# Optimization experiments

Measured on AMD Instinct MI355X. Metric: run time of the kernel, lower is better.

Reference implementation:

```python
import jax, jax.numpy as jnp
import numpy as np

N = 8192
IN_F = 512
OUT_F = 256
EDGE_P = 0.02  # adjacency density


def setup_inputs() -> dict:
    key = jax.random.key(0)
    k1, k2, k3, k4 = jax.random.split(key, 4)
    x = jax.random.normal(k1, (N, IN_F), dtype=jnp.float32)
    # xavier_uniform with gain=1.414 ~ std gain*sqrt(2/(fan_in+fan_out))
    W = jax.random.normal(k2, (IN_F, OUT_F), dtype=jnp.float32) * (1.414 * np.sqrt(2.0 / (IN_F + OUT_F)))
    a = jax.random.normal(k3, (2 * OUT_F, 1), dtype=jnp.float32) * (1.414 * np.sqrt(2.0 / (2 * OUT_F + 1)))
    adj = (jax.random.uniform(k4, (N, N)) < EDGE_P).astype(jnp.float32)
    return {"x": x, "adj": adj, "W": W, "a": a}


def reference(x, adj, W, a):
    h = x @ W                        # [N, F]
    F = h.shape[1]
    # repeat/cat reduces to an outer sum of two [N] vectors.
    s_src = (h @ a[:F]).squeeze(-1)  # [N], contribution of h_i
    s_dst = (h @ a[F:]).squeeze(-1)  # [N], contribution of h_j
    e = jax.nn.leaky_relu(s_src[:, None] + s_dst[None, :], negative_slope=0.2)  # [N, N]
    # NOTE: original code softmaxes over the FULL row, THEN multiplies by adj.
    attention = jax.nn.softmax(e, axis=1) * adj  # [N, N]
    h_prime = attention @ h                      # [N, F]
    return h_prime, attention
```

## Files before the change

### kernel.cpp

```cpp
#include <hip/hip_runtime.h>
#include <hip/hip_bf16.h>

#define N_NODES 8192
#define IN_F    512
#define OUT_F   256
#define MAXNZ   512

#define BM 64
#define BN 64
#define BK 32

typedef float v4f __attribute__((ext_vector_type(4)));

__global__ __launch_bounds__(256) void k_gemm_h(const float* __restrict__ x,
                                                const float* __restrict__ W,
                                                float* __restrict__ h) {
  __shared__ float As[BK][BM + 4];
  __shared__ float Bs[BK][BN];
  const int t  = threadIdx.x;
  const int bm = blockIdx.x >> 2;
  const int bn = blockIdx.x & 3;
  const int m0 = bm * BM, n0 = bn * BN;
  const int tm = (t >> 4) * 4;
  const int tn = (t & 15) * 4;

  float acc[4][4] = {{0.f, 0.f, 0.f, 0.f}, {0.f, 0.f, 0.f, 0.f},
                     {0.f, 0.f, 0.f, 0.f}, {0.f, 0.f, 0.f, 0.f}};

  for (int k0 = 0; k0 < IN_F; k0 += BK) {
#pragma unroll
    for (int i = 0; i < 2; ++i) {
      const int fi = t + i * 256;
      const int ar = fi >> 3;
      const int ac = (fi & 7) << 2;
      const float4 va = *(const float4*)&x[(size_t)(m0 + ar) * IN_F + k0 + ac];
      As[ac + 0][ar] = va.x;
      As[ac + 1][ar] = va.y;
      As[ac + 2][ar] = va.z;
      As[ac + 3][ar] = va.w;
      const int br = fi >> 4;
      const int bc = (fi & 15) << 2;
      *(float4*)&Bs[br][bc] = *(const float4*)&W[(size_t)(k0 + br) * OUT_F + n0 + bc];
    }
    __syncthreads();
#pragma unroll
    for (int k = 0; k < BK; ++k) {
      const float4 a = *(const float4*)&As[k][tm];
      const float4 b = *(const float4*)&Bs[k][tn];
      acc[0][0] = fmaf(a.x, b.x, acc[0][0]);
      acc[0][1] = fmaf(a.x, b.y, acc[0][1]);
      acc[0][2] = fmaf(a.x, b.z, acc[0][2]);
      acc[0][3] = fmaf(a.x, b.w, acc[0][3]);
      acc[1][0] = fmaf(a.y, b.x, acc[1][0]);
      acc[1][1] = fmaf(a.y, b.y, acc[1][1]);
      acc[1][2] = fmaf(a.y, b.z, acc[1][2]);
      acc[1][3] = fmaf(a.y, b.w, acc[1][3]);
      acc[2][0] = fmaf(a.z, b.x, acc[2][0]);
      acc[2][1] = fmaf(a.z, b.y, acc[2][1]);
      acc[2][2] = fmaf(a.z, b.z, acc[2][2]);
      acc[2][3] = fmaf(a.z, b.w, acc[2][3]);
      acc[3][0] = fmaf(a.w, b.x, acc[3][0]);
      acc[3][1] = fmaf(a.w, b.y, acc[3][1]);
      acc[3][2] = fmaf(a.w, b.z, acc[3][2]);
      acc[3][3] = fmaf(a.w, b.w, acc[3][3]);
    }
    __syncthreads();
  }
#pragma unroll
  for (int r = 0; r < 4; ++r) {
    float4 o;
    o.x = acc[r][0]; o.y = acc[r][1]; o.z = acc[r][2]; o.w = acc[r][3];
    *(float4*)&h[(size_t)(m0 + tm + r) * OUT_F + n0 + tn] = o;
  }
}

__global__ __launch_bounds__(256) void k_scores(const float* __restrict__ h,
                                                const float* __restrict__ a,
                                                float* __restrict__ s_src,
                                                float* __restrict__ s_dst) {
  const int row = blockIdx.x * 4 + (threadIdx.x >> 6);
  const int l   = threadIdx.x & 63;
  const float4 hv = ((const float4*)(h + (size_t)row * OUT_F))[l];
  const float4 a0 = ((const float4*)a)[l];
  const float4 a1 = ((const float4*)(a + OUT_F))[l];
  float p0 = hv.x * a0.x + hv.y * a0.y + hv.z * a0.z + hv.w * a0.w;
  float p1 = hv.x * a1.x + hv.y * a1.y + hv.z * a1.z + hv.w * a1.w;
#pragma unroll
  for (int off = 32; off > 0; off >>= 1) {
    p0 += __shfl_down(p0, off);
    p1 += __shfl_down(p1, off);
  }
  if (l == 0) { s_src[row] = p0; s_dst[row] = p1; }
}

__device__ __forceinline__ float lrelu_exp(float v) {
  const float e = v > 0.f ? v : 0.2f * v;
  return __expf(e);
}

__global__ __launch_bounds__(256) void k_attn(const float* __restrict__ adj,
                                              const float* __restrict__ h,
                                              const float* __restrict__ s_src,
                                              const float* __restrict__ s_dst,
                                              float* __restrict__ out_hp,
                                              float* __restrict__ out_att) {
  __shared__ float nza[MAXNZ];
  __shared__ int   nzj[MAXNZ];
  __shared__ float redbuf[4];
  __shared__ int   cnt;

  const int t = threadIdx.x;
  const int i = blockIdx.x;
  const float ssrc = s_src[i];
  if (t == 0) cnt = 0;

  const float4* sd4 = (const float4*)s_dst;
  float4 sd[8];
#pragma unroll
  for (int c = 0; c < 8; ++c) sd[c] = sd4[c * 256 + t];

  float lsum = 0.f;
#pragma unroll
  for (int c = 0; c < 8; ++c) {
    lsum += lrelu_exp(ssrc + sd[c].x) + lrelu_exp(ssrc + sd[c].y)
          + lrelu_exp(ssrc + sd[c].z) + lrelu_exp(ssrc + sd[c].w);
  }
#pragma unroll
  for (int off = 32; off > 0; off >>= 1) lsum += __shfl_down(lsum, off);
  if ((t & 63) == 0) redbuf[t >> 6] = lsum;
  __syncthreads();
  const float inv = 1.0f / (redbuf[0] + redbuf[1] + redbuf[2] + redbuf[3]);

  const v4f* adj4 = (const v4f*)(adj + (size_t)i * N_NODES);
  v4f*       att4 = (v4f*)(out_att + (size_t)i * N_NODES);
  v4f av[8];
#pragma unroll
  for (int c = 0; c < 8; ++c) av[c] = __builtin_nontemporal_load(adj4 + c * 256 + t);
#pragma unroll
  for (int c = 0; c < 8; ++c) {
    v4f att;
    att.x = av[c].x * (lrelu_exp(ssrc + sd[c].x) * inv);
    att.y = av[c].y * (lrelu_exp(ssrc + sd[c].y) * inv);
    att.z = av[c].z * (lrelu_exp(ssrc + sd[c].z) * inv);
    att.w = av[c].w * (lrelu_exp(ssrc + sd[c].w) * inv);
    __builtin_nontemporal_store(att, att4 + c * 256 + t);
    const int j = (c * 256 + t) * 4;
    if (av[c].x != 0.f) { const int k = atomicAdd(&cnt, 1); if (k < MAXNZ) { nzj[k] = j + 0; nza[k] = att.x; } }
    if (av[c].y != 0.f) { const int k = atomicAdd(&cnt, 1); if (k < MAXNZ) { nzj[k] = j + 1; nza[k] = att.y; } }
    if (av[c].z != 0.f) { const int k = atomicAdd(&cnt, 1); if (k < MAXNZ) { nzj[k] = j + 2; nza[k] = att.z; } }
    if (av[c].w != 0.f) { const int k = atomicAdd(&cnt, 1); if (k < MAXNZ) { nzj[k] = j + 3; nza[k] = att.w; } }
  }
  __syncthreads();

  const int n = cnt < MAXNZ ? cnt : MAXNZ;
  float acc = 0.f;
#pragma unroll 8
  for (int k = 0; k < n; ++k) {
    acc = fmaf(nza[k], h[(size_t)nzj[k] * OUT_F + t], acc);
  }
  out_hp[(size_t)i * OUT_F + t] = acc;
}

extern "C" void kernel_launch(void* const* d_in, const int* in_sizes, int n_in,
                              void* d_out, int out_size, void* d_ws, size_t ws_size,
                              hipStream_t stream) {
  const float* x   = (const float*)d_in[0];
  const float* adj = (const float*)d_in[1];
  const float* W   = (const float*)d_in[2];
  const float* a   = (const float*)d_in[3];

  float* out_hp  = (float*)d_out;
  float* out_att = (float*)d_out + (size_t)N_NODES * OUT_F;

  float* h_ws    = (float*)d_ws;
  float* ssrc_ws = h_ws + (size_t)N_NODES * OUT_F;
  float* sdst_ws = ssrc_ws + N_NODES;

  k_gemm_h<<<(N_NODES / BM) * (OUT_F / BN), 256, 0, stream>>>(x, W, h_ws);
  k_scores<<<N_NODES / 4, 256, 0, stream>>>(h_ws, a, ssrc_ws, sdst_ws);
  k_attn<<<N_NODES, 256, 0, stream>>>(adj, h_ws, ssrc_ws, sdst_ws, out_hp, out_att);
}
```

Measured before the change: 541.9 us.

## Use split-K larger-tile GEMM with atomic reduction and wave-ballot compaction

The h GEMM now uses 64x128 tiles with an 8x4 per-thread register tile and splits K in two, accumulating partial results into a zeroed buffer with float atomics. A memset is added before it. The attention kernel replaces per-element LDS atomics for nonzero compaction with a wave ballot, one atomic per wave, and a popcount prefix. The GEMM change raises arithmetic intensity per thread but adds a memset, global atomics and nondeterministic summation order. The compaction change cuts LDS atomic contention.

```diff
diff --git a/kernel.cpp b/kernel.cpp
--- a/kernel.cpp
+++ b/kernel.cpp
@@ -6,28 +6,35 @@
 #define OUT_F   256
 #define MAXNZ   512
 
-#define BM 64
-#define BN 64
-#define BK 32
+#define GBM 64
+#define GBN 128
+#define GBK 32
 
 typedef float v4f __attribute__((ext_vector_type(4)));
 
 __global__ __launch_bounds__(256) void k_gemm_h(const float* __restrict__ x,
                                                 const float* __restrict__ W,
                                                 float* __restrict__ h) {
-  __shared__ float As[BK][BM + 4];
-  __shared__ float Bs[BK][BN];
+  __shared__ float As[GBK][GBM + 4];
+  __shared__ float Bs[GBK][GBN + 4];
   const int t  = threadIdx.x;
+  const int ks = blockIdx.x & 1;
+  const int bn = (blockIdx.x >> 1) & 1;
   const int bm = blockIdx.x >> 2;
-  const int bn = blockIdx.x & 3;
-  const int m0 = bm * BM, n0 = bn * BN;
-  const int tm = (t >> 4) * 4;
-  const int tn = (t & 15) * 4;
-
-  float acc[4][4] = {{0.f, 0.f, 0.f, 0.f}, {0.f, 0.f, 0.f, 0.f},
-                     {0.f, 0.f, 0.f, 0.f}, {0.f, 0.f, 0.f, 0.f}};
-
-  for (int k0 = 0; k0 < IN_F; k0 += BK) {
+  const int m0 = bm * GBM, n0 = bn * GBN;
+  const int kbase = ks * (IN_F / 2);
+
+  const int mg = (t >> 3) & 7;
+  const int ng = (t & 7) | ((t >> 6) << 3);
+
+  float acc[8][4];
+#pragma unroll
+  for (int r = 0; r < 8; ++r)
+#pragma unroll
+    for (int c = 0; c < 4; ++c) acc[r][c] = 0.f;
+
+  for (int o = 0; o < IN_F / 2; o += GBK) {
+    const int k0 = kbase + o;
 #pragma unroll
     for (int i = 0; i < 2; ++i) {
       const int fi = t + i * 256;
@@ -38,39 +45,36 @@
       As[ac + 1][ar] = va.y;
       As[ac + 2][ar] = va.z;
       As[ac + 3][ar] = va.w;
-      const int br = fi >> 4;
-      const int bc = (fi & 15) << 2;
+    }
+#pragma unroll
+    for (int i = 0; i < 4; ++i) {
+      const int fi = t + i * 256;
+      const int br = fi >> 5;
+      const int bc = (fi & 31) << 2;
       *(float4*)&Bs[br][bc] = *(const float4*)&W[(size_t)(k0 + br) * OUT_F + n0 + bc];
     }
     __syncthreads();
 #pragma unroll
-    for (int k = 0; k < BK; ++k) {
-      const float4 a = *(const float4*)&As[k][tm];
-      const float4 b = *(const float4*)&Bs[k][tn];
-      acc[0][0] = fmaf(a.x, b.x, acc[0][0]);
-      acc[0][1] = fmaf(a.x, b.y, acc[0][1]);
-      acc[0][2] = fmaf(a.x, b.z, acc[0][2]);
-      acc[0][3] = fmaf(a.x, b.w, acc[0][3]);
-      acc[1][0] = fmaf(a.y, b.x, acc[1][0]);
-      acc[1][1] = fmaf(a.y, b.y, acc[1][1]);
-      acc[1][2] = fmaf(a.y, b.z, acc[1][2]);
-      acc[1][3] = fmaf(a.y, b.w, acc[1][3]);
-      acc[2][0] = fmaf(a.z, b.x, acc[2][0]);
-      acc[2][1] = fmaf(a.z, b.y, acc[2][1]);
-      acc[2][2] = fmaf(a.z, b.z, acc[2][2]);
-      acc[2][3] = fmaf(a.z, b.w, acc[2][3]);
-      acc[3][0] = fmaf(a.w, b.x, acc[3][0]);
-      acc[3][1] = fmaf(a.w, b.y, acc[3][1]);
-      acc[3][2] = fmaf(a.w, b.z, acc[3][2]);
-      acc[3][3] = fmaf(a.w, b.w, acc[3][3]);
+    for (int k = 0; k < GBK; ++k) {
+      const float4 a0 = *(const float4*)&As[k][mg * 8 + 0];
+      const float4 a1 = *(const float4*)&As[k][mg * 8 + 4];
+      const float4 b  = *(const float4*)&Bs[k][ng * 4];
+      const float ar[8] = {a0.x, a0.y, a0.z, a0.w, a1.x, a1.y, a1.z, a1.w};
+#pragma unroll
+      for (int r = 0; r < 8; ++r) {
+        acc[r][0] = fmaf(ar[r], b.x, acc[r][0]);
+        acc[r][1] = fmaf(ar[r], b.y, acc[r][1]);
+        acc[r][2] = fmaf(ar[r], b.z, acc[r][2]);
+        acc[r][3] = fmaf(ar[r], b.w, acc[r][3]);
+      }
     }
     __syncthreads();
   }
 #pragma unroll
-  for (int r = 0; r < 4; ++r) {
-    float4 o;
-    o.x = acc[r][0]; o.y = acc[r][1]; o.z = acc[r][2]; o.w = acc[r][3];
-    *(float4*)&h[(size_t)(m0 + tm + r) * OUT_F + n0 + tn] = o;
+  for (int r = 0; r < 8; ++r) {
+    float* hp = &h[(size_t)(m0 + mg * 8 + r) * OUT_F + n0 + ng * 4];
+#pragma unroll
+    for (int c = 0; c < 4; ++c) atomicAdd(hp + c, acc[r][c]);
   }
 }
 
@@ -109,8 +113,9 @@
   __shared__ float redbuf[4];
   __shared__ int   cnt;
 
-  const int t = threadIdx.x;
-  const int i = blockIdx.x;
+  const int t    = threadIdx.x;
+  const int lane = t & 63;
+  const int i    = blockIdx.x;
   const float ssrc = s_src[i];
   if (t == 0) cnt = 0;
 
@@ -127,7 +132,7 @@
   }
 #pragma unroll
   for (int off = 32; off > 0; off >>= 1) lsum += __shfl_down(lsum, off);
-  if ((t & 63) == 0) redbuf[t >> 6] = lsum;
+  if (lane == 0) redbuf[t >> 6] = lsum;
   __syncthreads();
   const float inv = 1.0f / (redbuf[0] + redbuf[1] + redbuf[2] + redbuf[3]);
 
@@ -136,6 +141,8 @@
   v4f av[8];
 #pragma unroll
   for (int c = 0; c < 8; ++c) av[c] = __builtin_nontemporal_load(adj4 + c * 256 + t);
+
+  const unsigned long long ltmask = (1ull << lane) - 1ull;
 #pragma unroll
   for (int c = 0; c < 8; ++c) {
     v4f att;
@@ -145,10 +152,22 @@
     att.w = av[c].w * (lrelu_exp(ssrc + sd[c].w) * inv);
     __builtin_nontemporal_store(att, att4 + c * 256 + t);
     const int j = (c * 256 + t) * 4;
-    if (av[c].x != 0.f) { const int k = atomicAdd(&cnt, 1); if (k < MAXNZ) { nzj[k] = j + 0; nza[k] = att.x; } }
-    if (av[c].y != 0.f) { const int k = atomicAdd(&cnt, 1); if (k < MAXNZ) { nzj[k] = j + 1; nza[k] = att.y; } }
-    if (av[c].z != 0.f) { const int k = atomicAdd(&cnt, 1); if (k < MAXNZ) { nzj[k] = j + 2; nza[k] = att.z; } }
-    if (av[c].w != 0.f) { const int k = atomicAdd(&cnt, 1); if (k < MAXNZ) { nzj[k] = j + 3; nza[k] = att.w; } }
+#define COMPACT(comp, idx)                                                        \
+    {                                                                             \
+      const unsigned long long m = __ballot(av[c].comp != 0.f);                   \
+      int b0 = 0;                                                                 \
+      if (lane == 0 && m) b0 = atomicAdd(&cnt, __popcll(m));                      \
+      b0 = __shfl(b0, 0);                                                         \
+      if (av[c].comp != 0.f) {                                                    \
+        const int pos = b0 + (int)__popcll(m & ltmask);                           \
+        if (pos < MAXNZ) { nzj[pos] = j + idx; nza[pos] = att.comp; }             \
+      }                                                                           \
+    }
+    COMPACT(x, 0)
+    COMPACT(y, 1)
+    COMPACT(z, 2)
+    COMPACT(w, 3)
+#undef COMPACT
   }
   __syncthreads();
 
@@ -176,7 +195,9 @@
   float* ssrc_ws = h_ws + (size_t)N_NODES * OUT_F;
   float* sdst_ws = ssrc_ws + N_NODES;
 
-  k_gemm_h<<<(N_NODES / BM) * (OUT_F / BN), 256, 0, stream>>>(x, W, h_ws);
+  hipMemsetAsync(h_ws, 0, (size_t)N_NODES * OUT_F * sizeof(float), stream);
+
+  k_gemm_h<<<(N_NODES / GBM) * (OUT_F / GBN) * 2, 256, 0, stream>>>(x, W, h_ws);
   k_scores<<<N_NODES / 4, 256, 0, stream>>>(h_ws, a, ssrc_ws, sdst_ws);
   k_attn<<<N_NODES, 256, 0, stream>>>(adj, h_ws, ssrc_ws, sdst_ws, out_hp, out_att);
 }
```

Result: slower. 589.2 us (+8.7%).

## Use split-bf16 MFMA for x@W and read bf16 h in sparse aggregation

Applied to the files above, without the earlier changes.

Replaces the fp32 SIMT GEMM with a bf16 MFMA GEMM. It splits x and W into hi/lo bf16 parts and runs three MFMAs per step to keep roughly fp32 accuracy, after separate cast kernels write the bf16 copies to workspace. The GEMM also emits a bf16 copy of h, which the attention kernel gathers instead of fp32 h to halve the bytes of the neighbour gather. The cost is two extra kernel launches plus extra traffic to cast x and W, and precision loss in h_prime from the bf16 h.

```diff
diff --git a/kernel.cpp b/kernel.cpp
--- a/kernel.cpp
+++ b/kernel.cpp
@@ -6,71 +6,95 @@
 #define OUT_F   256
 #define MAXNZ   512
 
-#define BM 64
-#define BN 64
-#define BK 32
-
-typedef float v4f __attribute__((ext_vector_type(4)));
-
-__global__ __launch_bounds__(256) void k_gemm_h(const float* __restrict__ x,
-                                                const float* __restrict__ W,
-                                                float* __restrict__ h) {
-  __shared__ float As[BK][BM + 4];
-  __shared__ float Bs[BK][BN];
-  const int t  = threadIdx.x;
-  const int bm = blockIdx.x >> 2;
-  const int bn = blockIdx.x & 3;
-  const int m0 = bm * BM, n0 = bn * BN;
-  const int tm = (t >> 4) * 4;
-  const int tn = (t & 15) * 4;
-
-  float acc[4][4] = {{0.f, 0.f, 0.f, 0.f}, {0.f, 0.f, 0.f, 0.f},
-                     {0.f, 0.f, 0.f, 0.f}, {0.f, 0.f, 0.f, 0.f}};
-
-  for (int k0 = 0; k0 < IN_F; k0 += BK) {
-#pragma unroll
-    for (int i = 0; i < 2; ++i) {
-      const int fi = t + i * 256;
-      const int ar = fi >> 3;
-      const int ac = (fi & 7) << 2;
-      const float4 va = *(const float4*)&x[(size_t)(m0 + ar) * IN_F + k0 + ac];
-      As[ac + 0][ar] = va.x;
-      As[ac + 1][ar] = va.y;
-      As[ac + 2][ar] = va.z;
-      As[ac + 3][ar] = va.w;
-      const int br = fi >> 4;
-      const int bc = (fi & 15) << 2;
-      *(float4*)&Bs[br][bc] = *(const float4*)&W[(size_t)(k0 + br) * OUT_F + n0 + bc];
+typedef float v4f  __attribute__((ext_vector_type(4)));
+typedef __attribute__((ext_vector_type(8)))  short bf16x8;
+typedef __attribute__((ext_vector_type(16))) float f32x16;
+typedef unsigned short u16;
+typedef unsigned int   u32;
+
+__device__ __forceinline__ u16 f2bf(float f) {
+  u32 u = __float_as_uint(f);
+  u += 0x7fffu + ((u >> 16) & 1u);
+  return (u16)(u >> 16);
+}
+__device__ __forceinline__ float bf2f(u16 h) {
+  return __uint_as_float(((u32)h) << 16);
+}
+
+__global__ __launch_bounds__(256) void k_cast_x(const float* __restrict__ x,
+                                                u16* __restrict__ x_hi,
+                                                u16* __restrict__ x_lo) {
+  const int idx = blockIdx.x * 256 + threadIdx.x;
+  const float4 v = ((const float4*)x)[idx];
+  u16 h0 = f2bf(v.x), h1 = f2bf(v.y), h2 = f2bf(v.z), h3 = f2bf(v.w);
+  u16 l0 = f2bf(v.x - bf2f(h0)), l1 = f2bf(v.y - bf2f(h1));
+  u16 l2 = f2bf(v.z - bf2f(h2)), l3 = f2bf(v.w - bf2f(h3));
+  uint2 hp, lp;
+  hp.x = (u32)h0 | ((u32)h1 << 16); hp.y = (u32)h2 | ((u32)h3 << 16);
+  lp.x = (u32)l0 | ((u32)l1 << 16); lp.y = (u32)l2 | ((u32)l3 << 16);
+  ((uint2*)x_hi)[idx] = hp;
+  ((uint2*)x_lo)[idx] = lp;
+}
+
+__global__ __launch_bounds__(256) void k_cast_wt(const float* __restrict__ W,
+                                                 u16* __restrict__ wt_hi,
+                                                 u16* __restrict__ wt_lo) {
+  const int k = blockIdx.x;
+  const int n = threadIdx.x;
+  const float v = W[(size_t)k * OUT_F + n];
+  const u16 h = f2bf(v);
+  wt_hi[(size_t)n * IN_F + k] = h;
+  wt_lo[(size_t)n * IN_F + k] = f2bf(v - bf2f(h));
+}
+
+__global__ __launch_bounds__(256) void k_gemm_mfma(const u16* __restrict__ x_hi,
+                                                   const u16* __restrict__ x_lo,
+                                                   const u16* __restrict__ wt_hi,
+                                                   const u16* __restrict__ wt_lo,
+                                                   float* __restrict__ h,
+                                                   u16* __restrict__ h_bf) {
+  __shared__ u16 As_hi[64 * 40], As_lo[64 * 40], Bs_hi[64 * 40], Bs_lo[64 * 40];
+  const int t    = threadIdx.x;
+  const int bn   = blockIdx.x & 3;
+  const int bm   = blockIdx.x >> 2;
+  const int m0   = bm * 64, n0 = bn * 64;
+  const int lane = t & 63;
+  const int w    = t >> 6;
+  const int wm   = w & 1, wn = w >> 1;
+
+  const int sm = t >> 2;
+  const int sk = (t & 3) * 8;
+
+  f32x16 acc = {};
+
+  for (int k0 = 0; k0 < IN_F; k0 += 32) {
+    *(bf16x8*)&As_hi[sm * 40 + sk] = *(const bf16x8*)&x_hi[(size_t)(m0 + sm) * IN_F + k0 + sk];
+    *(bf16x8*)&As_lo[sm * 40 + sk] = *(const bf16x8*)&x_lo[(size_t)(m0 + sm) * IN_F + k0 + sk];
+    *(bf16x8*)&Bs_hi[sm * 40 + sk] = *(const bf16x8*)&wt_hi[(size_t)(n0 + sm) * IN_F + k0 + sk];
+    *(bf16x8*)&Bs_lo[sm * 40 + sk] = *(const bf16x8*)&wt_lo[(size_t)(n0 + sm) * IN_F + k0 + sk];
+    __syncthreads();
+    const int am = wm * 32 + (lane & 31);
+    const int bn_ = wn * 32 + (lane & 31);
+#pragma unroll
+    for (int kk = 0; kk < 2; ++kk) {
+      const int ko = kk * 16 + (lane >> 5) * 8;
+      const bf16x8 ah = *(const bf16x8*)&As_hi[am * 40 + ko];
+      const bf16x8 al = *(const bf16x8*)&As_lo[am * 40 + ko];
+      const bf16x8 bh = *(const bf16x8*)&Bs_hi[bn_ * 40 + ko];
+      const bf16x8 bl = *(const bf16x8*)&Bs_lo[bn_ * 40 + ko];
+      acc = __builtin_amdgcn_mfma_f32_32x32x16_bf16(ah, bh, acc, 0, 0, 0);
+      acc = __builtin_amdgcn_mfma_f32_32x32x16_bf16(al, bh, acc, 0, 0, 0);
+      acc = __builtin_amdgcn_mfma_f32_32x32x16_bf16(ah, bl, acc, 0, 0, 0);
     }
     __syncthreads();
-#pragma unroll
-    for (int k = 0; k < BK; ++k) {
-      const float4 a = *(const float4*)&As[k][tm];
-      const float4 b = *(const float4*)&Bs[k][tn];
-      acc[0][0] = fmaf(a.x, b.x, acc[0][0]);
-      acc[0][1] = fmaf(a.x, b.y, acc[0][1]);
-      acc[0][2] = fmaf(a.x, b.z, acc[0][2]);
-      acc[0][3] = fmaf(a.x, b.w, acc[0][3]);
-      acc[1][0] = fmaf(a.y, b.x, acc[1][0]);
-      acc[1][1] = fmaf(a.y, b.y, acc[1][1]);
-      acc[1][2] = fmaf(a.y, b.z, acc[1][2]);
-      acc[1][3] = fmaf(a.y, b.w, acc[1][3]);
-      acc[2][0] = fmaf(a.z, b.x, acc[2][0]);
-      acc[2][1] = fmaf(a.z, b.y, acc[2][1]);
-      acc[2][2] = fmaf(a.z, b.z, acc[2][2]);
-      acc[2][3] = fmaf(a.z, b.w, acc[2][3]);
-      acc[3][0] = fmaf(a.w, b.x, acc[3][0]);
-      acc[3][1] = fmaf(a.w, b.y, acc[3][1]);
-      acc[3][2] = fmaf(a.w, b.z, acc[3][2]);
-      acc[3][3] = fmaf(a.w, b.w, acc[3][3]);
-    }
-    __syncthreads();
-  }
-#pragma unroll
-  for (int r = 0; r < 4; ++r) {
-    float4 o;
-    o.x = acc[r][0]; o.y = acc[r][1]; o.z = acc[r][2]; o.w = acc[r][3];
-    *(float4*)&h[(size_t)(m0 + tm + r) * OUT_F + n0 + tn] = o;
+  }
+  const int col = n0 + wn * 32 + (lane & 31);
+#pragma unroll
+  for (int r = 0; r < 16; ++r) {
+    const int row = m0 + wm * 32 + (r & 3) + 8 * (r >> 2) + 4 * (lane >> 5);
+    const float v = acc[r];
+    h[(size_t)row * OUT_F + col]    = v;
+    h_bf[(size_t)row * OUT_F + col] = f2bf(v);
   }
 }
 
@@ -99,7 +123,7 @@
 }
 
 __global__ __launch_bounds__(256) void k_attn(const float* __restrict__ adj,
-                                              const float* __restrict__ h,
+                                              const u16* __restrict__ h_bf,
                                               const float* __restrict__ s_src,
                                               const float* __restrict__ s_dst,
                                               float* __restrict__ out_hp,
@@ -156,7 +180,7 @@
   float acc = 0.f;
 #pragma unroll 8
   for (int k = 0; k < n; ++k) {
-    acc = fmaf(nza[k], h[(size_t)nzj[k] * OUT_F + t], acc);
+    acc = fmaf(nza[k], bf2f(h_bf[(size_t)nzj[k] * OUT_F + t]), acc);
   }
   out_hp[(size_t)i * OUT_F + t] = acc;
 }
@@ -172,11 +196,19 @@
   float* out_hp  = (float*)d_out;
   float* out_att = (float*)d_out + (size_t)N_NODES * OUT_F;
 
-  float* h_ws    = (float*)d_ws;
-  float* ssrc_ws = h_ws + (size_t)N_NODES * OUT_F;
-  float* sdst_ws = ssrc_ws + N_NODES;
-
-  k_gemm_h<<<(N_NODES / BM) * (OUT_F / BN), 256, 0, stream>>>(x, W, h_ws);
+  char* ws = (char*)d_ws;
+  float* h_ws    = (float*)ws;                       ws += (size_t)N_NODES * OUT_F * 4;
+  float* ssrc_ws = (float*)ws;                       ws += N_NODES * 4;
+  float* sdst_ws = (float*)ws;                       ws += N_NODES * 4;
+  u16*   x_hi    = (u16*)ws;                         ws += (size_t)N_NODES * IN_F * 2;
+  u16*   x_lo    = (u16*)ws;                         ws += (size_t)N_NODES * IN_F * 2;
+  u16*   wt_hi   = (u16*)ws;                         ws += (size_t)OUT_F * IN_F * 2;
+  u16*   wt_lo   = (u16*)ws;                         ws += (size_t)OUT_F * IN_F * 2;
+  u16*   h_bf    = (u16*)ws;                         ws += (size_t)N_NODES * OUT_F * 2;
+
+  k_cast_x<<<(N_NODES * IN_F / 4) / 256, 256, 0, stream>>>(x, x_hi, x_lo);
+  k_cast_wt<<<IN_F, OUT_F, 0, stream>>>(W, wt_hi, wt_lo);
+  k_gemm_mfma<<<(N_NODES / 64) * (OUT_F / 64), 256, 0, stream>>>(x_hi, x_lo, wt_hi, wt_lo, h_ws, h_bf);
   k_scores<<<N_NODES / 4, 256, 0, stream>>>(h_ws, a, ssrc_ws, sdst_ws);
-  k_attn<<<N_NODES, 256, 0, stream>>>(adj, h_ws, ssrc_ws, sdst_ws, out_hp, out_att);
-}
+  k_attn<<<N_NODES, 256, 0, stream>>>(adj, h_bf, ssrc_ws, sdst_ws, out_hp, out_att);
+}
```

New measurement: 509.9 us. -5.9%, faster.
